# Kernel optimization log

Measured on AMD Instinct MI355X. Metric: run time of the kernel, lower is better.

## Reference

```python
import jax, jax.numpy as jnp
import numpy as np

B, LATENT, HID, NL, MAXN, HEADS = 512, 128, 256, 2, 50, 4
TAU = 1.0
P = MAXN * (MAXN - 1) // 2  # 1225 upper-triangular pairs


def _gru_layer(x, w_ih, w_hh, b_ih, b_hh):
    # x: [B, T, in]; torch GRU gate order: r, z, n
    xg = jnp.einsum('bti,gi->btg', x, w_ih) + b_ih  # [B, T, 3H]
    H = w_hh.shape[1]

    def step(h, xg_t):
        hg = h @ w_hh.T + b_hh
        xr, xz, xn = jnp.split(xg_t, 3, axis=-1)
        hr, hz, hn = jnp.split(hg, 3, axis=-1)
        r = jax.nn.sigmoid(xr + hr)
        zt = jax.nn.sigmoid(xz + hz)
        n = jnp.tanh(xn + r * hn)
        h_new = (1.0 - zt) * n + zt * h
        return h_new, h_new

    h0 = jnp.zeros((x.shape[0], H), x.dtype)
    _, ys = jax.lax.scan(step, h0, jnp.swapaxes(xg, 0, 1))
    return jnp.swapaxes(ys, 0, 1)  # [B, T, H]


def setup_inputs() -> dict:
    key = jax.random.key(0)
    ks = jax.random.split(key, 24)
    s = 0.05
    inp = {
        'z': jax.random.normal(ks[0], (B, LATENT), jnp.float32),
        'n_nodes': jax.random.randint(ks[1], (B,), 1, MAXN + 1).astype(jnp.int32),
        'n_edges': 100,
        'pos_emb': jax.random.normal(ks[2], (MAXN, LATENT), jnp.float32),
        'w_ih0': s * jax.random.normal(ks[3], (3 * HID, LATENT), jnp.float32),
        'w_hh0': s * jax.random.normal(ks[4], (3 * HID, HID), jnp.float32),
        'b_ih0': s * jax.random.normal(ks[5], (3 * HID,), jnp.float32),
        'b_hh0': s * jax.random.normal(ks[6], (3 * HID,), jnp.float32),
        'w_ih1': s * jax.random.normal(ks[7], (3 * HID, HID), jnp.float32),
        'w_hh1': s * jax.random.normal(ks[8], (3 * HID, HID), jnp.float32),
        'b_ih1': s * jax.random.normal(ks[9], (3 * HID,), jnp.float32),
        'b_hh1': s * jax.random.normal(ks[10], (3 * HID,), jnp.float32),
        'node_proj_w': s * jax.random.normal(ks[11], (HID, HID), jnp.float32),
        'attn_in_w': s * jax.random.normal(ks[12], (3 * HID, HID), jnp.float32),
        'attn_in_b': s * jax.random.normal(ks[13], (3 * HID,), jnp.float32),
        'attn_out_w': s * jax.random.normal(ks[14], (HID, HID), jnp.float32),
        'attn_out_b': s * jax.random.normal(ks[15], (HID,), jnp.float32),
        'mlp_w1': s * jax.random.normal(ks[16], (HID, HID), jnp.float32),
        'mlp_b1': s * jax.random.normal(ks[17], (HID,), jnp.float32),
        'mlp_w2': s * jax.random.normal(ks[18], (2, HID), jnp.float32),
        'mlp_b2': s * jax.random.normal(ks[19], (2,), jnp.float32),
    }
    u = jax.random.uniform(ks[20], (B, P, 2), jnp.float32, 1e-6, 1.0 - 1e-6)
    inp['gumbel_noise'] = -jnp.log(-jnp.log(u))
    return inp


def reference(z, n_nodes, n_edges, pos_emb, w_ih0, w_hh0, b_ih0, b_hh0,
              w_ih1, w_hh1, b_ih1, b_hh1, node_proj_w, attn_in_w, attn_in_b,
              attn_out_w, attn_out_b, mlp_w1, mlp_b1, mlp_w2, mlp_b2,
              gumbel_noise):
    Bz = z.shape[0]
    N = pos_emb.shape[0]
    H = w_hh0.shape[1]
    # broadcast latent + positional embeddings, zero padded positions
    seq = z[:, None, :] + pos_emb[None, :, :]                    # [B, N, L]
    mask = jnp.arange(N)[None, :] < n_nodes[:, None]             # [B, N]
    seq = seq * mask[..., None].astype(seq.dtype)
    # 2-layer GRU; packing == valid prefixes, so full run + output masking
    h = _gru_layer(seq, w_ih0, w_hh0, b_ih0, b_hh0)
    h = _gru_layer(h, w_ih1, w_hh1, b_ih1, b_hh1)
    rnn_out = h * mask[..., None].astype(h.dtype)
    node_emb = jnp.einsum('bnh,oh->bno', rnn_out, node_proj_w)   # [B, N, H]
    iu, ju = jnp.triu_indices(N, k=1)
    emb_i = node_emb[:, iu, :]                                   # [B, P, H]
    emb_j = node_emb[:, ju, :]
    # tiny per-pair MHA: 1 query, 2 keys
    wq, wk, wv = jnp.split(attn_in_w, 3, axis=0)
    bq, bk, bv = jnp.split(attn_in_b, 3)
    q = emb_i @ wq.T + bq                                        # [B, P, H]
    kv = jnp.stack([emb_i, emb_j], axis=2)                       # [B, P, 2, H]
    k = kv @ wk.T + bk
    v = kv @ wv.T + bv
    hd = H // HEADS
    Pn = q.shape[1]
    qh = q.reshape(Bz, Pn, HEADS, hd)
    kh = k.reshape(Bz, Pn, 2, HEADS, hd)
    vh = v.reshape(Bz, Pn, 2, HEADS, hd)
    scores = jnp.einsum('bphd,bpkhd->bphk', qh, kh) / jnp.sqrt(
        jnp.asarray(hd, q.dtype))
    attn = jax.nn.softmax(scores, axis=-1)
    out = jnp.einsum('bphk,bpkhd->bphd', attn, vh).reshape(Bz, Pn, H)
    pair_emb = out @ attn_out_w.T + attn_out_b
    # MLP -> 2 logits per pair
    hid = jax.nn.relu(pair_emb @ mlp_w1.T + mlp_b1)
    logits = hid @ mlp_w2.T + mlp_b2                             # [B, P, 2]
    # hard gumbel-softmax (straight-through)
    y_soft = jax.nn.softmax((logits + gumbel_noise) / TAU, axis=-1)
    y_hard = jax.nn.one_hot(jnp.argmax(y_soft, axis=-1), 2, dtype=y_soft.dtype)
    y = jax.lax.stop_gradient(y_hard - y_soft) + y_soft
    vals = y[..., 0]                                             # [B, P]
    adj = jnp.zeros((Bz, N, N), z.dtype).at[:, iu, ju].set(vals)
    adj = adj + jnp.swapaxes(adj, 1, 2)
    mask2d = (mask[:, :, None] & mask[:, None, :]).astype(adj.dtype)
    return adj * mask2d
```

## Files before the change

kernel.cpp:

```cpp
#include <hip/hip_runtime.h>
#include <hip/hip_bf16.h>
#include <math.h>

#define BB 512
#define LATENT 128
#define HID 256
#define GDIM 768
#define NMAX 50
#define NHEADS 4
#define HD 64
#define NPAIRS 1225

__global__ __launch_bounds__(512) void k_offs(const int* __restrict__ nn,
                                              int* __restrict__ offs)
{
    __shared__ int s[512];
    const int tid = threadIdx.x;
    s[tid] = nn[tid];
    __syncthreads();
    for (int d = 1; d < 512; d <<= 1) {
        int v = (tid >= d) ? s[tid - d] : 0;
        __syncthreads();
        s[tid] += v;
        __syncthreads();
    }
    if (tid == 0) offs[0] = 0;
    offs[tid + 1] = s[tid];
}

template<int KD, bool XF64, bool OF64, bool BIAS, bool NLIVE>
__global__ __launch_bounds__(256) void k_gemm5(
        const void* __restrict__ Xv, long xstride, int xzoff,
        const int* __restrict__ nlivep,
        const float* __restrict__ W, int wstride, long wzoff,
        const float* __restrict__ bias,
        void* __restrict__ Ov, long ostride, int ozoff)
{
    const int rb = blockIdx.x * 64;
    if (NLIVE) { if (rb >= *nlivep) return; }
    __shared__ double xs[2][64][17];
    __shared__ float  wsm[2][128][17];
    const int ob = blockIdx.y * 128;
    const int zid = blockIdx.z;
    const int tid = threadIdx.x;
    const int ty = tid >> 4, tx = tid & 15;
    const int lr  = tid >> 2;
    const int lk  = (tid & 3) * 4;
    const int lr2 = tid >> 1;
    const int lk2 = (tid & 1) * 8;
    const int xrow = rb + lr;

    const double* xp64 = nullptr; const float* xp32 = nullptr;
    if (XF64) xp64 = (const double*)Xv + (size_t)xrow * xstride + zid * (long)xzoff;
    else      xp32 = (const float*)Xv + (size_t)xrow * xstride + zid * (long)xzoff;
    const float* wp = W + (size_t)zid * wzoff + (size_t)(ob + lr2) * wstride + lk2;

    double xstg[4]; float wstg[8];

#define GEMM_LOAD(K0)                                                          \
    {                                                                          \
        if (XF64) {                                                            \
            _Pragma("unroll")                                                  \
            for (int u = 0; u < 4; ++u) xstg[u] = xp64[(K0) + lk + u];         \
        } else {                                                               \
            _Pragma("unroll")                                                  \
            for (int u = 0; u < 4; ++u) xstg[u] = (double)xp32[(K0) + lk + u]; \
        }                                                                      \
        _Pragma("unroll")                                                      \
        for (int u = 0; u < 8; ++u) wstg[u] = wp[(K0) + u];                    \
    }

#define GEMM_WRITE(BUF)                                                        \
    {                                                                          \
        _Pragma("unroll")                                                      \
        for (int u = 0; u < 4; ++u) xs[(BUF)][lr][lk + u] = xstg[u];           \
        _Pragma("unroll")                                                      \
        for (int u = 0; u < 8; ++u) wsm[(BUF)][lr2][lk2 + u] = wstg[u];        \
    }

    double acc[4][8];
    #pragma unroll
    for (int i = 0; i < 4; ++i)
        #pragma unroll
        for (int j = 0; j < 8; ++j) acc[i][j] = 0.0;

    constexpr int NC = KD / 16;
    GEMM_LOAD(0);
    GEMM_WRITE(0);
    for (int c = 0; c < NC; ++c) {
        __syncthreads();
        if (c + 1 < NC) GEMM_LOAD((c + 1) * 16);
        const int bi = c & 1;
        #pragma unroll
        for (int kk = 0; kk < 16; ++kk) {
            double wv[8];
            #pragma unroll
            for (int j = 0; j < 8; ++j) wv[j] = (double)wsm[bi][j * 16 + tx][kk];
            #pragma unroll
            for (int i = 0; i < 4; ++i) {
                double xr = xs[bi][ty * 4 + i][kk];
                #pragma unroll
                for (int j = 0; j < 8; ++j) acc[i][j] += xr * wv[j];
            }
        }
        if (c + 1 < NC) GEMM_WRITE((c + 1) & 1);
    }
    #pragma unroll
    for (int i = 0; i < 4; ++i) {
        size_t row = rb + ty * 4 + i;
        #pragma unroll
        for (int j = 0; j < 8; ++j) {
            int ocg = ob + j * 16 + tx;
            double v = acc[i][j];
            if (BIAS) v += (double)bias[ocg];
            size_t o = row * ostride + (size_t)zid * ozoff + ocg;
            if (OF64) ((double*)Ov)[o] = v;
            else      ((float*)Ov)[o] = (float)v;
        }
    }
#undef GEMM_LOAD
#undef GEMM_WRITE
}

__global__ __launch_bounds__(256) void k_ap(
        const float* __restrict__ pos, const float* __restrict__ w,
        double* __restrict__ Ap)
{
    __shared__ float ps[LATENT];
    const int t = blockIdx.x;
    const int tid = threadIdx.x;
    if (tid < LATENT) ps[tid] = pos[(size_t)t * LATENT + tid];
    __syncthreads();
    for (int g = tid; g < GDIM; g += 256) {
        double acc = 0.0;
        const float* wr = w + (size_t)g * LATENT;
        for (int i = 0; i < LATENT; ++i) acc += (double)ps[i] * (double)wr[i];
        Ap[(size_t)t * GDIM + g] = acc;
    }
}

__global__ __launch_bounds__(256) void k_pack_bat(
        const float* __restrict__ whh, float2* __restrict__ wRZ,
        float* __restrict__ wN)
{
    int k = blockIdx.x, f = threadIdx.x;
    float r = whh[(size_t)(0 * HID + f) * HID + k];
    float zz = whh[(size_t)(1 * HID + f) * HID + k];
    float n = whh[(size_t)(2 * HID + f) * HID + k];
    wRZ[(size_t)k * HID + f] = make_float2(r, zz);
    wN[(size_t)k * HID + f] = n;
}

template<int XGMODE>
__global__ __launch_bounds__(1024) void k_gru8(
        const double* __restrict__ xg,
        const double* __restrict__ Ap,
        const float* __restrict__ bih,
        const int* __restrict__ nn,
        const int* __restrict__ offs,
        double* __restrict__ hout,
        const float2* __restrict__ wRZ, const float* __restrict__ wN,
        const float* __restrict__ bhh)
{
    const int tid = threadIdx.x;
    const int f  = tid & 255;
    const int kq = tid >> 8;
    const int b0 = blockIdx.x * 2;

    __shared__ double hs[HID][2];
    __shared__ double red[4][6][HID];

    if (kq < 2) hs[f][kq] = 0.0;

    const int nn0 = nn[b0], nn1 = nn[b0 + 1];
    const int tmax = nn0 > nn1 ? nn0 : nn1;

    const int bq = kq;
    const int bg = b0 + (kq < 2 ? kq : 0);
    const int nnb = (kq == 0) ? nn0 : ((kq == 1) ? nn1 : 0);
    const int offs_bg = offs[bg];
    double br = 0, bz = 0, bn = 0, bihr = 0, bihz = 0, bihn = 0;
    if (kq < 2) {
        br = (double)bhh[f]; bz = (double)bhh[HID + f]; bn = (double)bhh[2 * HID + f];
        if (XGMODE == 1) {
            bihr = (double)bih[f]; bihz = (double)bih[HID + f]; bihn = (double)bih[2 * HID + f];
        }
    }
    const float2* wrz = wRZ + (size_t)(kq * 64) * HID + f;
    const float*  wn  = wN  + (size_t)(kq * 64) * HID + f;
    const double* xbase = (XGMODE == 1)
        ? xg + (size_t)bg * GDIM + f
        : xg + (size_t)offs_bg * GDIM + f;
    double* hob = hout + (size_t)offs_bg * HID + f;
    const int kbase = kq * 64;

    __syncthreads();

    for (int t = 0; t < tmax; ++t) {
        const bool act = (kq < 2) && (t < nnb);
        double xr = 0, xz = 0, xn_ = 0;
        if (act) {
            if (XGMODE == 0) {
                const double* x = xbase + (size_t)t * GDIM;
                xr = x[0]; xz = x[HID]; xn_ = x[2 * HID];
            } else {
                const double* ap = Ap + (size_t)t * GDIM + f;
                xr  = xbase[0]       + ap[0]       + bihr;
                xz  = xbase[HID]     + ap[HID]     + bihz;
                xn_ = xbase[2 * HID] + ap[2 * HID] + bihn;
            }
        }

        double a0 = 0, a1 = 0, a2 = 0, a3 = 0, a4 = 0, a5 = 0;
        #pragma unroll 8
        for (int kk = 0; kk < 64; ++kk) {
            float2 rz = wrz[(size_t)kk * HID];
            float  nw = wn[(size_t)kk * HID];
            double wrd = (double)rz.x, wzd = (double)rz.y, wnd = (double)nw;
            double h0 = hs[kbase + kk][0], h1 = hs[kbase + kk][1];
            a0 += h0 * wrd; a1 += h1 * wrd;
            a2 += h0 * wzd; a3 += h1 * wzd;
            a4 += h0 * wnd; a5 += h1 * wnd;
        }
        red[kq][0][f] = a0; red[kq][1][f] = a1;
        red[kq][2][f] = a2; red[kq][3][f] = a3;
        red[kq][4][f] = a4; red[kq][5][f] = a5;
        __syncthreads();

        if (act) {
            double ar = 0, az = 0, an = 0;
            #pragma unroll
            for (int qq = 0; qq < 4; ++qq) {
                ar += red[qq][0 * 2 + bq][f];
                az += red[qq][1 * 2 + bq][f];
                an += red[qq][2 * 2 + bq][f];
            }
            double hp = hs[f][bq];
            double rg = 1.0 / (1.0 + exp(-(xr + ar + br)));
            double zg = 1.0 / (1.0 + exp(-(xz + az + bz)));
            double ng = tanh(xn_ + rg * (an + bn));
            double hn = (1.0 - zg) * ng + zg * hp;
            hs[f][bq] = hn;
            hob[(size_t)t * HID] = hn;
        }
        __syncthreads();
    }
}

__global__ __launch_bounds__(256) void k_wq(
        const float* __restrict__ aiw, const float* __restrict__ proj,
        float* __restrict__ WQ)
{
    __shared__ float arow[HID];
    int g = blockIdx.x, h = threadIdx.x;
    arow[h] = aiw[(size_t)g * HID + h];
    __syncthreads();
    double acc = 0.0;
    for (int o = 0; o < HID; ++o) acc += (double)arow[o] * (double)proj[(size_t)o * HID + h];
    WQ[(size_t)g * HID + h] = (float)acc;
}

__global__ __launch_bounds__(256) void k_m(
        const float* __restrict__ wo, const float* __restrict__ w1,
        float* __restrict__ M)
{
    __shared__ float w1row[HID];
    int k = blockIdx.x, hd = threadIdx.x;
    w1row[hd] = w1[(size_t)k * HID + hd];
    __syncthreads();
    double acc = 0.0;
    for (int m = 0; m < HID; ++m) acc += (double)w1row[m] * (double)wo[(size_t)m * HID + hd];
    M[(((size_t)(hd >> 6)) * HID + k) * HD + (hd & 63)] = (float)acc;
}

__global__ void k_const(const float* __restrict__ ob, const float* __restrict__ w1,
                        const float* __restrict__ b1, double* __restrict__ c)
{
    int k = threadIdx.x;
    double acc = 0.0;
    for (int m = 0; m < HID; ++m) acc += (double)ob[m] * (double)w1[k * HID + m];
    c[k] = acc + (double)b1[k];
}

__global__ __launch_bounds__(256) void k_pairs3(
        const float* __restrict__ QKV, const float* __restrict__ G,
        const double* __restrict__ c,
        const int* __restrict__ nn, const int* __restrict__ offs,
        const float* __restrict__ gum,
        const float* __restrict__ w2, const float* __restrict__ b2,
        float* __restrict__ adj)
{
    const int bi = blockIdx.x;
    const int b = bi / (NMAX - 1);
    const int i = bi % (NMAX - 1);
    const int nnb = nn[b];
    if (i >= nnb - 1) return;
    const int tid = threadIdx.x;
    const int lane = tid & 63;
    const int wave = tid >> 6;
    const int ofb = offs[b];
    const size_t rowi = (size_t)(ofb + i);

    double cw[4], w2r[4];
    float gir[4][4];
    #pragma unroll
    for (int q = 0; q < 4; ++q) {
        int k = lane + 64 * q;
        cw[q] = c[k];
        w2r[q] = (double)w2[k] - (double)w2[HID + k];
        #pragma unroll
        for (int h = 0; h < 4; ++h) gir[q][h] = G[rowi * 1024 + h * HID + k];
    }
    const int sh = lane >> 4, sd = (lane & 15) * 4;
    const float4 qv  = *(const float4*)&QKV[rowi * GDIM + sh * HD + sd];
    const float4 kv0 = *(const float4*)&QKV[rowi * GDIM + HID + sh * HD + sd];
    double s0 = (double)qv.x * kv0.x + (double)qv.y * kv0.y
              + (double)qv.z * kv0.z + (double)qv.w * kv0.w;
    #pragma unroll
    for (int m = 1; m < 16; m <<= 1) s0 += __shfl_xor(s0, m, 64);
    s0 *= 0.125;
    const double b2d = (double)b2[0] - (double)b2[1];

    for (int j = i + 1 + wave; j < nnb; j += 4) {
        const size_t rowj = (size_t)(ofb + j);
        const float4 kv = *(const float4*)&QKV[rowj * GDIM + HID + sh * HD + sd];
        double s1 = (double)qv.x * kv.x + (double)qv.y * kv.y
                  + (double)qv.z * kv.z + (double)qv.w * kv.w;
        #pragma unroll
        for (int m = 1; m < 16; m <<= 1) s1 += __shfl_xor(s1, m, 64);
        s1 *= 0.125;
        double mx = fmax(s0, s1);
        double e0 = exp(s0 - mx), e1 = exp(s1 - mx);
        double inv = 1.0 / (e0 + e1);
        double a0 = e0 * inv, a1 = e1 * inv;
        double a0h[4], a1h[4];
        #pragma unroll
        for (int h = 0; h < 4; ++h) {
            a0h[h] = __shfl(a0, h * 16, 64);
            a1h[h] = __shfl(a1, h * 16, 64);
        }
        double dsum = 0.0;
        #pragma unroll
        for (int q = 0; q < 4; ++q) {
            int k = lane + 64 * q;
            double pre = cw[q];
            #pragma unroll
            for (int h = 0; h < 4; ++h)
                pre += a0h[h] * (double)gir[q][h]
                     + a1h[h] * (double)G[rowj * 1024 + h * HID + k];
            if (pre > 0.0) dsum += pre * w2r[q];
        }
        #pragma unroll
        for (int m = 1; m < 64; m <<= 1) dsum += __shfl_xor(dsum, m, 64);
        if (lane == 0) {
            int p_idx = i * (2 * NMAX - i - 1) / 2 + (j - i - 1);
            const float* gp = gum + ((size_t)b * NPAIRS + p_idx) * 2;
            double d = dsum + b2d + (double)gp[0] - (double)gp[1];
            if (d >= 0.0) {
                adj[(size_t)b * NMAX * NMAX + i * NMAX + j] = 1.0f;
                adj[(size_t)b * NMAX * NMAX + j * NMAX + i] = 1.0f;
            }
        }
    }
}

__global__ void k_ws_too_small(float* adj) { adj[0] = 2.0f; }

extern "C" void kernel_launch(void* const* d_in, const int* in_sizes, int n_in,
                              void* d_out, int out_size, void* d_ws, size_t ws_size,
                              hipStream_t stream)
{
    const float* z          = (const float*)d_in[0];
    const int*   nn         = (const int*)d_in[1];
    const float* pos        = (const float*)d_in[3];
    const float* w_ih0      = (const float*)d_in[4];
    const float* w_hh0      = (const float*)d_in[5];
    const float* b_ih0      = (const float*)d_in[6];
    const float* b_hh0      = (const float*)d_in[7];
    const float* w_ih1      = (const float*)d_in[8];
    const float* w_hh1      = (const float*)d_in[9];
    const float* b_ih1      = (const float*)d_in[10];
    const float* b_hh1      = (const float*)d_in[11];
    const float* proj       = (const float*)d_in[12];
    const float* attn_in_w  = (const float*)d_in[13];
    const float* attn_in_b  = (const float*)d_in[14];
    const float* attn_out_w = (const float*)d_in[15];
    const float* attn_out_b = (const float*)d_in[16];
    const float* mlp_w1     = (const float*)d_in[17];
    const float* mlp_b1     = (const float*)d_in[18];
    const float* mlp_w2     = (const float*)d_in[19];
    const float* mlp_b2     = (const float*)d_in[20];
    const float* gum        = (const float*)d_in[21];

    float* adj = (float*)d_out;
    hipMemsetAsync(adj, 0, (size_t)out_size * sizeof(float), stream);

    const size_t NEED = 215795712;
    if (ws_size < NEED) { hipLaunchKernelGGL(k_ws_too_small, dim3(1), dim3(1), 0, stream, adj); return; }

    char* ws = (char*)d_ws;
    int*    offs = (int*)(ws);
    double* xg   = (double*)(ws + 4096);
    double* h01  = (double*)(ws + 157290496);
    float2* wRZ0 = (float2*)(ws + 209719296);
    float*  wN0  = (float*)(ws + 210243584);
    float2* wRZ1 = (float2*)(ws + 210505728);
    float*  wN1  = (float*)(ws + 211030016);
    float*  WQ   = (float*)(ws + 211292160);
    float*  M    = (float*)(ws + 212078592);
    double* cbf  = (double*)(ws + 212340736);
    double* Az   = (double*)(ws + 212342784);
    double* Ap   = (double*)(ws + 215488512);
    float*  qkv  = (float*)(ws + 4096);
    float*  G    = (float*)(ws + 78647296);
    const int* nlivep = offs + 512;

    hipLaunchKernelGGL(k_offs, dim3(1), dim3(512), 0, stream, nn, offs);
    hipLaunchKernelGGL((k_gemm5<LATENT, false, true, false, false>), dim3(8, 6), dim3(256), 0, stream,
                       (const void*)z, (long)LATENT, 0, nullptr,
                       w_ih0, LATENT, 0L, (const float*)nullptr,
                       (void*)Az, (long)GDIM, 0);
    hipLaunchKernelGGL(k_ap, dim3(NMAX), dim3(256), 0, stream, pos, w_ih0, Ap);
    hipLaunchKernelGGL(k_pack_bat, dim3(256), dim3(256), 0, stream, w_hh0, wRZ0, wN0);
    hipLaunchKernelGGL((k_gru8<1>), dim3(256), dim3(1024), 0, stream,
                       Az, Ap, b_ih0, nn, offs, h01, wRZ0, wN0, b_hh0);
    hipLaunchKernelGGL((k_gemm5<HID, true, true, true, true>), dim3(400, 6), dim3(256), 0, stream,
                       (const void*)h01, (long)HID, 0, nlivep,
                       w_ih1, HID, 0L, b_ih1, (void*)xg, (long)GDIM, 0);
    hipLaunchKernelGGL(k_pack_bat, dim3(256), dim3(256), 0, stream, w_hh1, wRZ1, wN1);
    hipLaunchKernelGGL((k_gru8<0>), dim3(256), dim3(1024), 0, stream,
                       xg, nullptr, nullptr, nn, offs, h01, wRZ1, wN1, b_hh1);
    hipLaunchKernelGGL(k_wq, dim3(768), dim3(256), 0, stream, attn_in_w, proj, WQ);
    hipLaunchKernelGGL((k_gemm5<HID, true, false, true, true>), dim3(400, 6), dim3(256), 0, stream,
                       (const void*)h01, (long)HID, 0, nlivep,
                       WQ, HID, 0L, attn_in_b, (void*)qkv, (long)GDIM, 0);
    hipLaunchKernelGGL(k_m, dim3(256), dim3(256), 0, stream, attn_out_w, mlp_w1, M);
    hipLaunchKernelGGL(k_const, dim3(1), dim3(256), 0, stream, attn_out_b, mlp_w1, mlp_b1, cbf);
    hipLaunchKernelGGL((k_gemm5<HD, false, false, false, true>), dim3(400, 2, 4), dim3(256), 0, stream,
                       (const void*)(qkv + 2 * HID), (long)GDIM, HD, nlivep,
                       M, HD, (long)(HID * HD), (const float*)nullptr,
                       (void*)G, 1024L, HID);
    hipLaunchKernelGGL(k_pairs3, dim3(BB * (NMAX - 1)), dim3(256), 0, stream,
                       qkv, G, cbf, nn, offs, gum, mlp_w2, mlp_b2, adj);
}
```

Baseline: 1.790 ms.

## Stream GRU recurrent weights through double-buffered LDS with one thread per gate column

```diff
diff --git a/kernel.cpp b/kernel.cpp
--- a/kernel.cpp
+++ b/kernel.cpp
@@ -139,111 +139,112 @@
     }
 }
 
-__global__ __launch_bounds__(256) void k_pack_bat(
-        const float* __restrict__ whh, float2* __restrict__ wRZ,
-        float* __restrict__ wN)
-{
-    int k = blockIdx.x, f = threadIdx.x;
-    float r = whh[(size_t)(0 * HID + f) * HID + k];
-    float zz = whh[(size_t)(1 * HID + f) * HID + k];
-    float n = whh[(size_t)(2 * HID + f) * HID + k];
-    wRZ[(size_t)k * HID + f] = make_float2(r, zz);
-    wN[(size_t)k * HID + f] = n;
+__global__ __launch_bounds__(256) void k_pack_all(
+        const float* __restrict__ whh, float* __restrict__ wAll)
+{
+    int idx = blockIdx.x * 256 + threadIdx.x;
+    int k = idx / GDIM, col = idx % GDIM;
+    wAll[idx] = whh[(size_t)col * HID + k];
 }
 
 template<int XGMODE>
-__global__ __launch_bounds__(1024) void k_gru8(
+__global__ __launch_bounds__(768) void k_gru10(
         const double* __restrict__ xg,
         const double* __restrict__ Ap,
         const float* __restrict__ bih,
         const int* __restrict__ nn,
         const int* __restrict__ offs,
         double* __restrict__ hout,
-        const float2* __restrict__ wRZ, const float* __restrict__ wN,
-        const float* __restrict__ bhh)
+        const float* __restrict__ wAll, const float* __restrict__ bhh)
 {
     const int tid = threadIdx.x;
-    const int f  = tid & 255;
-    const int kq = tid >> 8;
+    const int gf = tid & 255;
+    const int gb = tid >> 8;
     const int b0 = blockIdx.x * 2;
 
     __shared__ double hs[HID][2];
-    __shared__ double red[4][6][HID];
-
-    if (kq < 2) hs[f][kq] = 0.0;
+    __shared__ double red[3][2][HID];
+    __shared__ float  wbuf[2][16 * GDIM];
+
+    if (tid < 512) hs[gf][gb] = 0.0;
 
     const int nn0 = nn[b0], nn1 = nn[b0 + 1];
     const int tmax = nn0 > nn1 ? nn0 : nn1;
 
-    const int bq = kq;
-    const int bg = b0 + (kq < 2 ? kq : 0);
-    const int nnb = (kq == 0) ? nn0 : ((kq == 1) ? nn1 : 0);
-    const int offs_bg = offs[bg];
+    int nnb = 0;
     double br = 0, bz = 0, bn = 0, bihr = 0, bihz = 0, bihn = 0;
-    if (kq < 2) {
-        br = (double)bhh[f]; bz = (double)bhh[HID + f]; bn = (double)bhh[2 * HID + f];
+    const double* xbase = nullptr;
+    double* hob = nullptr;
+    if (tid < 512) {
+        const int bg = b0 + gb;
+        nnb = (gb == 0) ? nn0 : nn1;
+        br = (double)bhh[gf]; bz = (double)bhh[HID + gf]; bn = (double)bhh[2 * HID + gf];
         if (XGMODE == 1) {
-            bihr = (double)bih[f]; bihz = (double)bih[HID + f]; bihn = (double)bih[2 * HID + f];
-        }
-    }
-    const float2* wrz = wRZ + (size_t)(kq * 64) * HID + f;
-    const float*  wn  = wN  + (size_t)(kq * 64) * HID + f;
-    const double* xbase = (XGMODE == 1)
-        ? xg + (size_t)bg * GDIM + f
-        : xg + (size_t)offs_bg * GDIM + f;
-    double* hob = hout + (size_t)offs_bg * HID + f;
-    const int kbase = kq * 64;
-
-    __syncthreads();
+            bihr = (double)bih[gf]; bihz = (double)bih[HID + gf]; bihn = (double)bih[2 * HID + gf];
+            xbase = xg + (size_t)bg * GDIM + gf;
+        } else {
+            xbase = xg + (size_t)offs[bg] * GDIM + gf;
+        }
+        hob = hout + (size_t)offs[bg] * HID + gf;
+    }
+
+    const float4* wsrc = (const float4*)wAll;
+    float4 stg[4];
+    #pragma unroll
+    for (int r = 0; r < 4; ++r) stg[r] = wsrc[r * 768 + tid];
+    #pragma unroll
+    for (int r = 0; r < 4; ++r) ((float4*)&wbuf[0][0])[r * 768 + tid] = stg[r];
 
     for (int t = 0; t < tmax; ++t) {
-        const bool act = (kq < 2) && (t < nnb);
+        const bool act = (tid < 512) && (t < nnb);
         double xr = 0, xz = 0, xn_ = 0;
         if (act) {
             if (XGMODE == 0) {
                 const double* x = xbase + (size_t)t * GDIM;
                 xr = x[0]; xz = x[HID]; xn_ = x[2 * HID];
             } else {
-                const double* ap = Ap + (size_t)t * GDIM + f;
+                const double* ap = Ap + (size_t)t * GDIM + gf;
                 xr  = xbase[0]       + ap[0]       + bihr;
                 xz  = xbase[HID]     + ap[HID]     + bihz;
                 xn_ = xbase[2 * HID] + ap[2 * HID] + bihn;
             }
         }
 
-        double a0 = 0, a1 = 0, a2 = 0, a3 = 0, a4 = 0, a5 = 0;
-        #pragma unroll 8
-        for (int kk = 0; kk < 64; ++kk) {
-            float2 rz = wrz[(size_t)kk * HID];
-            float  nw = wn[(size_t)kk * HID];
-            double wrd = (double)rz.x, wzd = (double)rz.y, wnd = (double)nw;
-            double h0 = hs[kbase + kk][0], h1 = hs[kbase + kk][1];
-            a0 += h0 * wrd; a1 += h1 * wrd;
-            a2 += h0 * wzd; a3 += h1 * wzd;
-            a4 += h0 * wnd; a5 += h1 * wnd;
-        }
-        red[kq][0][f] = a0; red[kq][1][f] = a1;
-        red[kq][2][f] = a2; red[kq][3][f] = a3;
-        red[kq][4][f] = a4; red[kq][5][f] = a5;
+        double a0 = 0.0, a1 = 0.0;
+        for (int c = 0; c < 16; ++c) {
+            __syncthreads();
+            const int cn = (c + 1) & 15;
+            #pragma unroll
+            for (int r = 0; r < 4; ++r) stg[r] = wsrc[cn * 3072 + r * 768 + tid];
+            const float* wb = &wbuf[c & 1][0];
+            const int k0 = c * 16;
+            #pragma unroll
+            for (int kk = 0; kk < 16; ++kk) {
+                double w = (double)wb[kk * GDIM + tid];
+                double2 hv = *(const double2*)&hs[k0 + kk][0];
+                a0 += hv.x * w;
+                a1 += hv.y * w;
+            }
+            #pragma unroll
+            for (int r = 0; r < 4; ++r)
+                ((float4*)&wbuf[(c + 1) & 1][0])[r * 768 + tid] = stg[r];
+        }
+        red[gb][0][gf] = a0;
+        red[gb][1][gf] = a1;
         __syncthreads();
 
         if (act) {
-            double ar = 0, az = 0, an = 0;
-            #pragma unroll
-            for (int qq = 0; qq < 4; ++qq) {
-                ar += red[qq][0 * 2 + bq][f];
-                az += red[qq][1 * 2 + bq][f];
-                an += red[qq][2 * 2 + bq][f];
-            }
-            double hp = hs[f][bq];
+            double ar = red[0][gb][gf];
+            double az = red[1][gb][gf];
+            double an = red[2][gb][gf];
+            double hp = hs[gf][gb];
             double rg = 1.0 / (1.0 + exp(-(xr + ar + br)));
             double zg = 1.0 / (1.0 + exp(-(xz + az + bz)));
             double ng = tanh(xn_ + rg * (an + bn));
             double hn = (1.0 - zg) * ng + zg * hp;
-            hs[f][bq] = hn;
+            hs[gf][gb] = hn;
             hob[(size_t)t * HID] = hn;
         }
-        __syncthreads();
     }
 }
 
@@ -399,20 +400,18 @@
     if (ws_size < NEED) { hipLaunchKernelGGL(k_ws_too_small, dim3(1), dim3(1), 0, stream, adj); return; }
 
     char* ws = (char*)d_ws;
-    int*    offs = (int*)(ws);
-    double* xg   = (double*)(ws + 4096);
-    double* h01  = (double*)(ws + 157290496);
-    float2* wRZ0 = (float2*)(ws + 209719296);
-    float*  wN0  = (float*)(ws + 210243584);
-    float2* wRZ1 = (float2*)(ws + 210505728);
-    float*  wN1  = (float*)(ws + 211030016);
-    float*  WQ   = (float*)(ws + 211292160);
-    float*  M    = (float*)(ws + 212078592);
-    double* cbf  = (double*)(ws + 212340736);
-    double* Az   = (double*)(ws + 212342784);
-    double* Ap   = (double*)(ws + 215488512);
-    float*  qkv  = (float*)(ws + 4096);
-    float*  G    = (float*)(ws + 78647296);
+    int*    offs  = (int*)(ws);
+    double* xg    = (double*)(ws + 4096);
+    double* h01   = (double*)(ws + 157290496);
+    float*  wAll0 = (float*)(ws + 209719296);
+    float*  wAll1 = (float*)(ws + 210505728);
+    float*  WQ    = (float*)(ws + 211292160);
+    float*  M     = (float*)(ws + 212078592);
+    double* cbf   = (double*)(ws + 212340736);
+    double* Az    = (double*)(ws + 212342784);
+    double* Ap    = (double*)(ws + 215488512);
+    float*  qkv   = (float*)(ws + 4096);
+    float*  G     = (float*)(ws + 78647296);
     const int* nlivep = offs + 512;
 
     hipLaunchKernelGGL(k_offs, dim3(1), dim3(512), 0, stream, nn, offs);
@@ -421,15 +420,15 @@
                        w_ih0, LATENT, 0L, (const float*)nullptr,
                        (void*)Az, (long)GDIM, 0);
     hipLaunchKernelGGL(k_ap, dim3(NMAX), dim3(256), 0, stream, pos, w_ih0, Ap);
-    hipLaunchKernelGGL(k_pack_bat, dim3(256), dim3(256), 0, stream, w_hh0, wRZ0, wN0);
-    hipLaunchKernelGGL((k_gru8<1>), dim3(256), dim3(1024), 0, stream,
-                       Az, Ap, b_ih0, nn, offs, h01, wRZ0, wN0, b_hh0);
+    hipLaunchKernelGGL(k_pack_all, dim3(768), dim3(256), 0, stream, w_hh0, wAll0);
+    hipLaunchKernelGGL((k_gru10<1>), dim3(256), dim3(768), 0, stream,
+                       Az, Ap, b_ih0, nn, offs, h01, wAll0, b_hh0);
     hipLaunchKernelGGL((k_gemm5<HID, true, true, true, true>), dim3(400, 6), dim3(256), 0, stream,
                        (const void*)h01, (long)HID, 0, nlivep,
                        w_ih1, HID, 0L, b_ih1, (void*)xg, (long)GDIM, 0);
-    hipLaunchKernelGGL(k_pack_bat, dim3(256), dim3(256), 0, stream, w_hh1, wRZ1, wN1);
-    hipLaunchKernelGGL((k_gru8<0>), dim3(256), dim3(1024), 0, stream,
-                       xg, nullptr, nullptr, nn, offs, h01, wRZ1, wN1, b_hh1);
+    hipLaunchKernelGGL(k_pack_all, dim3(768), dim3(256), 0, stream, w_hh1, wAll1);
+    hipLaunchKernelGGL((k_gru10<0>), dim3(256), dim3(768), 0, stream,
+                       xg, nullptr, nullptr, nn, offs, h01, wAll1, b_hh1);
     hipLaunchKernelGGL(k_wq, dim3(768), dim3(256), 0, stream, attn_in_w, proj, WQ);
     hipLaunchKernelGGL((k_gemm5<HID, true, false, true, true>), dim3(400, 6), dim3(256), 0, stream,
                        (const void*)h01, (long)HID, 0, nlivep,
```

Result: slower. 2.428 ms (+35.6%).
